# Kernel optimization log

Hardware: AMD Instinct MI355X
Metric: run time of the kernel (lower is better)

Reference implementation:

```python
import jax, jax.numpy as jnp
import numpy as np

NEG_SLOPE = 0.2

def gatv2(x, edge_index, Wl, bl, Wr, br, att, bias):
    # PyG GATv2Conv (share_weights=False, add_self_loops=True, concat=True)
    N = x.shape[0]
    H, D = att.shape
    src0, dst0 = edge_index[0], edge_index[1]
    # remove_self_loops + add_self_loops semantics: mask existing self loops,
    # append one self loop per node (keeps static shapes under jit)
    loop = jnp.arange(N, dtype=src0.dtype)
    src = jnp.concatenate([src0, loop])
    dst = jnp.concatenate([dst0, loop])
    keep = jnp.concatenate([src0 != dst0, jnp.ones(N, dtype=bool)])  # drop original i->i edges
    xl = (x @ Wl + bl).reshape(N, H, D)  # source-side transform
    xr = (x @ Wr + br).reshape(N, H, D)  # target-side transform
    e = xl[src] + xr[dst]                                  # [E,H,D]
    logits = jnp.einsum('ehd,hd->eh', jax.nn.leaky_relu(e, NEG_SLOPE), att)
    logits = jnp.where(keep[:, None], logits, -jnp.inf)
    m = jax.ops.segment_max(logits, dst, num_segments=N)   # [N,H]
    ex = jnp.where(keep[:, None], jnp.exp(logits - m[dst]), 0.0)
    denom = jax.ops.segment_sum(ex, dst, num_segments=N)   # [N,H]
    alpha = ex / (denom[dst] + 1e-16)                      # [E,H]
    out = jax.ops.segment_sum(alpha[..., None] * xl[src], dst, num_segments=N)
    return out.reshape(N, H * D) + bias

def setup_inputs() -> dict:
    key = jax.random.key(0)
    ks = jax.random.split(key, 20)
    N, E, F, Hd = 50000, 400000, 5, 128
    s = 0.05
    inp = {
        'x': jax.random.normal(ks[0], (N, F), dtype=jnp.float32),
        'edge_index': jax.random.randint(ks[1], (2, E), 0, N, dtype=jnp.int64),
        # node_embed MLP
        'W1': jax.random.normal(ks[2], (F, Hd), dtype=jnp.float32) * s,
        'b1': jnp.zeros((Hd,), jnp.float32),
        'W2': jax.random.normal(ks[3], (Hd, Hd), dtype=jnp.float32) * s,
        'b2': jnp.zeros((Hd,), jnp.float32),
        # gnn1: GATv2Conv(128 -> 128, heads=4)
        'Wl1': jax.random.normal(ks[4], (Hd, 4 * Hd), dtype=jnp.float32) * s,
        'bl1': jnp.zeros((4 * Hd,), jnp.float32),
        'Wr1': jax.random.normal(ks[5], (Hd, 4 * Hd), dtype=jnp.float32) * s,
        'br1': jnp.zeros((4 * Hd,), jnp.float32),
        'att1': jax.random.normal(ks[6], (4, Hd), dtype=jnp.float32) * s,
        'bias1': jnp.zeros((4 * Hd,), jnp.float32),
        # gnn2: GATv2Conv(512 -> 128, heads=1)
        'Wl2': jax.random.normal(ks[7], (4 * Hd, Hd), dtype=jnp.float32) * s,
        'bl2': jnp.zeros((Hd,), jnp.float32),
        'Wr2': jax.random.normal(ks[8], (4 * Hd, Hd), dtype=jnp.float32) * s,
        'br2': jnp.zeros((Hd,), jnp.float32),
        'att2': jax.random.normal(ks[9], (1, Hd), dtype=jnp.float32) * s,
        'bias2': jnp.zeros((Hd,), jnp.float32),
    }
    return inp

def reference(x, edge_index, W1, b1, W2, b2, Wl1, bl1, Wr1, br1, att1, bias1,
              Wl2, bl2, Wr2, br2, att2, bias2):
    h = jax.nn.relu(x @ W1 + b1) @ W2 + b2                 # node_embed MLP
    h = jax.nn.relu(gatv2(h, edge_index, Wl1, bl1, Wr1, br1, att1, bias1))
    out = gatv2(h, edge_index, Wl2, bl2, Wr2, br2, att2, bias2)
    return out  # [N, 128]
```

## Files before the change

kernel.cpp:

```cpp
#include <hip/hip_runtime.h>
#include <math.h>

typedef __attribute__((ext_vector_type(8))) short bf16x8;
typedef __attribute__((ext_vector_type(4))) float f32x4;
typedef unsigned short ushort;
typedef unsigned int uint;

static __device__ __forceinline__ ushort f2bf(float f) {
    unsigned u = __float_as_uint(f);
    u = u + 0x7fff + ((u >> 16) & 1);
    return (ushort)(u >> 16);
}
static __device__ __forceinline__ float bf2f(ushort h) {
    return __uint_as_float(((unsigned)h) << 16);
}

template <int CTRL>
static __device__ __forceinline__ float dpp_add(float c) {
    int p = __builtin_amdgcn_update_dpp(0, __float_as_int(c), CTRL, 0xf, 0xf, true);
    return c + __int_as_float(p);
}
static __device__ __forceinline__ float group16_sum(float c) {
    c = dpp_add<0xB1>(c);
    c = dpp_add<0x4E>(c);
    c = dpp_add<0x141>(c);
    c = dpp_add<0x140>(c);
    return c;
}


__global__ void k_fill(const int* __restrict__ src, const int* __restrict__ dst,
                       int E, int* __restrict__ counts, int* __restrict__ colA) {
    int i = blockIdx.x * blockDim.x + threadIdx.x;
    if (i < E) {
        int s = src[i], d = dst[i];
        if (s != d) {
            int p = atomicAdd(&counts[d], 1);
            if (p < 64) colA[(size_t)d * 64 + p] = s;
        }
    }
}


__global__ __launch_bounds__(256) void k_repack(
    const float* __restrict__ W2, const float* __restrict__ Wl1,
    const float* __restrict__ Wr1, const float* __restrict__ Wl2,
    const float* __restrict__ Wr2,
    ushort* __restrict__ wfh, ushort* __restrict__ wfl)
{
    int job = blockIdx.y;
    int t = blockIdx.x * 256 + threadIdx.x;
    int ks = t >> 9, n = (t >> 6) & 7, l = t & 63;

    const float* W; int ldw, rowoff, col0;
    if (job == 0)      { W = W2;  ldw = 128; rowoff = 0;              col0 = 0; }
    else if (job < 5)  { W = Wl1; ldw = 512; rowoff = 0;              col0 = (job - 1) * 128; }
    else if (job < 9)  { W = Wr1; ldw = 512; rowoff = 0;              col0 = (job - 5) * 128; }
    else if (job < 13) { W = Wl2; ldw = 128; rowoff = (job - 9) * 128;  col0 = 0; }
    else               { W = Wr2; ldw = 128; rowoff = (job - 13) * 128; col0 = 0; }

    int krow = rowoff + ks * 32 + (l >> 4) * 8;
    int col = col0 + n * 16 + (l & 15);
    size_t dbase = (size_t)job * 16384 + (((size_t)(ks * 8 + n)) * 64 + l) * 8;
#pragma unroll
    for (int j = 0; j < 8; j++) {
        float v = W[(size_t)(krow + j) * ldw + col];
        ushort h = f2bf(v);
        ushort lo = f2bf(v - bf2f(h));
        wfh[dbase + j] = h;
        wfl[dbase + j] = lo;
    }
}


__global__ __launch_bounds__(256) void k_mlp_h0(
    const float* __restrict__ x, const float* __restrict__ W1, const float* __restrict__ b1,
    const ushort* __restrict__ wfh, const ushort* __restrict__ wfl,
    const float* __restrict__ b2,
    ushort* __restrict__ C, int M)
{
    int tid = threadIdx.x;
    int w = tid >> 6, l = tid & 63;
    int m0 = blockIdx.x * 128 + w * 32;
    int lr = l & 15, kg = l >> 4;

    int row0 = m0 + lr, row1 = row0 + 16;
    bool ok0 = row0 < M, ok1 = row1 < M;

    float x0[5], x1[5];
#pragma unroll
    for (int k = 0; k < 5; k++) {
        x0[k] = ok0 ? x[(size_t)row0 * 5 + k] : 0.f;
        x1[k] = ok1 ? x[(size_t)row1 * 5 + k] : 0.f;
    }

    bf16x8 a0[4], a1[4];
#pragma unroll
    for (int ks = 0; ks < 4; ks++) {
#pragma unroll
        for (int j = 0; j < 8; j++) {
            int col = ks * 32 + kg * 8 + j;
            float wc[5];
#pragma unroll
            for (int k = 0; k < 5; k++) wc[k] = W1[k * 128 + col];
            float bb = b1[col];
            float h0v = bb, h1v = bb;
#pragma unroll
            for (int k = 0; k < 5; k++) {
                h0v = fmaf(x0[k], wc[k], h0v);
                h1v = fmaf(x1[k], wc[k], h1v);
            }
            a0[ks][j] = (short)f2bf(fmaxf(h0v, 0.f));
            a1[ks][j] = (short)f2bf(fmaxf(h1v, 0.f));
        }
    }

    f32x4 acc[2][8];
#pragma unroll
    for (int i = 0; i < 2; i++)
#pragma unroll
        for (int j = 0; j < 8; j++) acc[i][j] = (f32x4){0.f, 0.f, 0.f, 0.f};

#pragma unroll
    for (int ks = 0; ks < 4; ks++) {
#pragma unroll
        for (int n = 0; n < 8; n++) {
            size_t bo = (((size_t)(ks * 8 + n)) * 64 + l) * 8;
            bf16x8 bh = *(const bf16x8*)(wfh + bo);
            bf16x8 bl = *(const bf16x8*)(wfl + bo);
            acc[0][n] = __builtin_amdgcn_mfma_f32_16x16x32_bf16(a0[ks], bh, acc[0][n], 0, 0, 0);
            acc[0][n] = __builtin_amdgcn_mfma_f32_16x16x32_bf16(a0[ks], bl, acc[0][n], 0, 0, 0);
            acc[1][n] = __builtin_amdgcn_mfma_f32_16x16x32_bf16(a1[ks], bh, acc[1][n], 0, 0, 0);
            acc[1][n] = __builtin_amdgcn_mfma_f32_16x16x32_bf16(a1[ks], bl, acc[1][n], 0, 0, 0);
        }
    }

#pragma unroll
    for (int mf = 0; mf < 2; mf++) {
#pragma unroll
        for (int r = 0; r < 4; r++) {
            int row = m0 + mf * 16 + kg * 4 + r;
            if (row >= M) continue;
#pragma unroll
            for (int n = 0; n < 8; n++) {
                size_t idx = (size_t)row * 128 + n * 16 + lr;
                C[idx] = f2bf(acc[mf][n][r] + b2[n * 16 + lr]);
            }
        }
    }
}


__global__ __launch_bounds__(256) void gemm_xlr1(
    const ushort* __restrict__ A,
    const ushort* __restrict__ wh, const ushort* __restrict__ wl,
    const float* __restrict__ bl1, const float* __restrict__ br1,
    ushort* __restrict__ out, int M)
{
    int tid = threadIdx.x;
    int w = tid >> 6, l = tid & 63;
    int m0 = blockIdx.x * 128 + w * 32;
    int lr = l & 15, kg = l >> 4;

    int row0 = m0 + lr, row1 = row0 + 16;
    bool ok0 = row0 < M, ok1 = row1 < M;
    const bf16x8 zz = {0, 0, 0, 0, 0, 0, 0, 0};

    bf16x8 a0[4], a1[4];
#pragma unroll
    for (int ks = 0; ks < 4; ks++) {
        int koff = ks * 32 + kg * 8;
        a0[ks] = ok0 ? *(const bf16x8*)(A + (size_t)row0 * 128 + koff) : zz;
        a1[ks] = ok1 ? *(const bf16x8*)(A + (size_t)row1 * 128 + koff) : zz;
    }

    for (int t = 0; t < 8; t++) {
        const ushort* bh_base = wh + (size_t)t * 16384;
        const ushort* bl_base = wl + (size_t)t * 16384;

        f32x4 acc[2][8];
#pragma unroll
        for (int i = 0; i < 2; i++)
#pragma unroll
            for (int j = 0; j < 8; j++) acc[i][j] = (f32x4){0.f, 0.f, 0.f, 0.f};

#pragma unroll
        for (int ks = 0; ks < 4; ks++) {
#pragma unroll
            for (int n = 0; n < 8; n++) {
                size_t bo = (((size_t)(ks * 8 + n)) * 64 + l) * 8;
                bf16x8 bh = *(const bf16x8*)(bh_base + bo);
                bf16x8 bl = *(const bf16x8*)(bl_base + bo);
                acc[0][n] = __builtin_amdgcn_mfma_f32_16x16x32_bf16(a0[ks], bh, acc[0][n], 0, 0, 0);
                acc[0][n] = __builtin_amdgcn_mfma_f32_16x16x32_bf16(a0[ks], bl, acc[0][n], 0, 0, 0);
                acc[1][n] = __builtin_amdgcn_mfma_f32_16x16x32_bf16(a1[ks], bh, acc[1][n], 0, 0, 0);
                acc[1][n] = __builtin_amdgcn_mfma_f32_16x16x32_bf16(a1[ks], bl, acc[1][n], 0, 0, 0);
            }
        }

        float bcol[8];
#pragma unroll
        for (int n = 0; n < 8; n++)
            bcol[n] = (t < 4) ? bl1[t * 128 + n * 16 + lr] : br1[(t - 4) * 128 + n * 16 + lr];

#pragma unroll
        for (int mf = 0; mf < 2; mf++) {
#pragma unroll
            for (int r = 0; r < 4; r++) {
                int row = m0 + mf * 16 + kg * 4 + r;
                if (row >= M) continue;
#pragma unroll
                for (int n = 0; n < 8; n++)
                    out[(size_t)row * 1024 + t * 128 + n * 16 + lr] = f2bf(acc[mf][n][r] + bcol[n]);
            }
        }
    }
}


__global__ __launch_bounds__(256) void gemm_xlr2(
    const ushort* __restrict__ A,
    const ushort* __restrict__ wfh, const ushort* __restrict__ wfl,
    const float* __restrict__ bl2, const float* __restrict__ br2,
    ushort* __restrict__ xl2, ushort* __restrict__ xr2, int M)
{
    int tid = threadIdx.x;
    int w = tid >> 6, l = tid & 63;
    int m0 = blockIdx.x * 64 + w * 16;
    int lr = l & 15, kg = l >> 4;

    int row0 = m0 + lr;
    bool ok0 = row0 < M;
    const bf16x8 zz = {0, 0, 0, 0, 0, 0, 0, 0};

    f32x4 acc[2][8];
#pragma unroll
    for (int i = 0; i < 2; i++)
#pragma unroll
        for (int j = 0; j < 8; j++) acc[i][j] = (f32x4){0.f, 0.f, 0.f, 0.f};

    for (int kc = 0; kc < 4; kc++) {
        bf16x8 ah[4];
#pragma unroll
        for (int ks = 0; ks < 4; ks++)
            ah[ks] = ok0 ? *(const bf16x8*)(A + (size_t)row0 * 512 + kc * 128 + ks * 32 + kg * 8) : zz;

#pragma unroll
        for (int t = 0; t < 2; t++) {
            const ushort* bh_base = wfh + (size_t)(9 + t * 4 + kc) * 16384;
            const ushort* bl_base = wfl + (size_t)(9 + t * 4 + kc) * 16384;
#pragma unroll
            for (int ks = 0; ks < 4; ks++) {
#pragma unroll
                for (int n = 0; n < 8; n++) {
                    size_t bo = (((size_t)(ks * 8 + n)) * 64 + l) * 8;
                    bf16x8 bh = *(const bf16x8*)(bh_base + bo);
                    bf16x8 bl = *(const bf16x8*)(bl_base + bo);
                    acc[t][n] = __builtin_amdgcn_mfma_f32_16x16x32_bf16(ah[ks], bh, acc[t][n], 0, 0, 0);
                    acc[t][n] = __builtin_amdgcn_mfma_f32_16x16x32_bf16(ah[ks], bl, acc[t][n], 0, 0, 0);
                }
            }
        }
    }

#pragma unroll
    for (int r = 0; r < 4; r++) {
        int row = m0 + kg * 4 + r;
        if (row >= M) continue;
#pragma unroll
        for (int n = 0; n < 8; n++) {
            int col = n * 16 + lr;
            xl2[(size_t)row * 128 + col] = f2bf(acc[0][n][r] + bl2[col]);
            xr2[(size_t)row * 128 + col] = f2bf(acc[1][n][r] + br2[col]);
        }
    }
}


__global__ __launch_bounds__(256) void gat_edge4(
    const ushort* __restrict__ xlr,
    const float* __restrict__ att,
    const float* __restrict__ bias,
    const int* __restrict__ counts, const int* __restrict__ colA,
    ushort* __restrict__ h1,
    int N)
{
    int n = blockIdx.x;
    int h = threadIdx.x >> 6, l = threadIdx.x & 63;
    int g = l >> 4, q = l & 15;

    const ushort* xlbase = xlr + h * 128 + q * 8;

    bf16x8 xrv = *(const bf16x8*)(xlr + (size_t)n * 1024 + (4 + h) * 128 + q * 8);
    float4 ata = *(const float4*)(att + h * 128 + q * 8);
    float4 atb = *(const float4*)(att + h * 128 + q * 8 + 4);
    float xr[8] , at[8] = {ata.x, ata.y, ata.z, ata.w, atb.x, atb.y, atb.z, atb.w};
#pragma unroll
    for (int j = 0; j < 8; j++) xr[j] = bf2f((ushort)xrv[j]);

    auto dotc = [&](bf16x8 v8, float* vv) -> float {
        float c = 0.f;
#pragma unroll
        for (int j = 0; j < 8; j++) {
            vv[j] = bf2f((ushort)v8[j]);
            float t = vv[j] + xr[j];
            t = (t > 0.f) ? t : 0.2f * t;
            c = fmaf(t, at[j], c);
        }
        return group16_sum(c);
    };

    float selfv[8];
    bf16x8 vself = *(const bf16x8*)(xlbase + (size_t)n * 1024);
    float cs = dotc(vself, selfv);

    int cnt = min(counts[n], 64);
    const int* col = colA + (size_t)n * 64;

    float s = 0.f, o[8];
#pragma unroll
    for (int j = 0; j < 8; j++) o[j] = 0.f;

    auto edge = [&](bf16x8 v8) {
        float vv[8];
        float c = dotc(v8, vv);
        float p = __expf(fminf(c - cs, 80.f));
        s += p;
#pragma unroll
        for (int j = 0; j < 8; j++) o[j] = fmaf(p, vv[j], o[j]);
    };

    for (int base = g; base < cnt; base += 16) {
        int x0 = col[base];
        int x1 = (base + 4  < cnt) ? col[base + 4]  : -1;
        int x2 = (base + 8  < cnt) ? col[base + 8]  : -1;
        int x3 = (base + 12 < cnt) ? col[base + 12] : -1;
        int y1 = (x1 >= 0) ? x1 : n;
        int y2 = (x2 >= 0) ? x2 : n;
        int y3 = (x3 >= 0) ? x3 : n;
        bf16x8 v0 = *(const bf16x8*)(xlbase + (size_t)x0 * 1024);
        bf16x8 v1 = *(const bf16x8*)(xlbase + (size_t)y1 * 1024);
        bf16x8 v2 = *(const bf16x8*)(xlbase + (size_t)y2 * 1024);
        bf16x8 v3 = *(const bf16x8*)(xlbase + (size_t)y3 * 1024);
        edge(v0);
        if (x1 >= 0) edge(v1);
        if (x2 >= 0) edge(v2);
        if (x3 >= 0) edge(v3);
    }

#pragma unroll
    for (int off = 16; off <= 32; off <<= 1) {
        s += __shfl_xor(s, off);
#pragma unroll
        for (int j = 0; j < 8; j++) o[j] += __shfl_xor(o[j], off);
    }

    s += 1.f;
#pragma unroll
    for (int j = 0; j < 8; j++) o[j] += selfv[j];

    if (g == 0) {
        float inv = 1.f / (s + 1e-16f);
        float4 ba = *(const float4*)(bias + h * 128 + q * 8);
        float4 bb = *(const float4*)(bias + h * 128 + q * 8 + 4);
        float bs[8] = {ba.x, ba.y, ba.z, ba.w, bb.x, bb.y, bb.z, bb.w};
        bf16x8 pk;
#pragma unroll
        for (int j = 0; j < 8; j++)
            pk[j] = (short)f2bf(fmaxf(o[j] * inv + bs[j], 0.f));
        *(bf16x8*)(h1 + (size_t)n * 512 + h * 128 + q * 8) = pk;
    }
}


__global__ __launch_bounds__(256) void gat_edge1(
    const ushort* __restrict__ xl, const ushort* __restrict__ xr,
    const float* __restrict__ att, const float* __restrict__ bias,
    const int* __restrict__ counts, const int* __restrict__ colA,
    float* __restrict__ out, int N)
{
    int n = blockIdx.x * 4 + (threadIdx.x >> 6);
    if (n >= N) return;
    int l = threadIdx.x & 63;
    int g = l >> 4, q = l & 15;

    const ushort* xlbase = xl + q * 8;

    bf16x8 xrv = *(const bf16x8*)(xr + (size_t)n * 128 + q * 8);
    float4 ata = *(const float4*)(att + q * 8);
    float4 atb = *(const float4*)(att + q * 8 + 4);
    float xrr[8], at[8] = {ata.x, ata.y, ata.z, ata.w, atb.x, atb.y, atb.z, atb.w};
#pragma unroll
    for (int j = 0; j < 8; j++) xrr[j] = bf2f((ushort)xrv[j]);

    auto dotc = [&](bf16x8 v8, float* vv) -> float {
        float c = 0.f;
#pragma unroll
        for (int j = 0; j < 8; j++) {
            vv[j] = bf2f((ushort)v8[j]);
            float t = vv[j] + xrr[j];
            t = (t > 0.f) ? t : 0.2f * t;
            c = fmaf(t, at[j], c);
        }
        return group16_sum(c);
    };

    float selfv[8];
    bf16x8 vself = *(const bf16x8*)(xlbase + (size_t)n * 128);
    float cs = dotc(vself, selfv);

    int cnt = min(counts[n], 64);
    const int* col = colA + (size_t)n * 64;

    float s = 0.f, o[8];
#pragma unroll
    for (int j = 0; j < 8; j++) o[j] = 0.f;

    auto edge = [&](bf16x8 v8) {
        float vv[8];
        float c = dotc(v8, vv);
        float p = __expf(fminf(c - cs, 80.f));
        s += p;
#pragma unroll
        for (int j = 0; j < 8; j++) o[j] = fmaf(p, vv[j], o[j]);
    };

    for (int base = g; base < cnt; base += 16) {
        int x0 = col[base];
        int x1 = (base + 4  < cnt) ? col[base + 4]  : -1;
        int x2 = (base + 8  < cnt) ? col[base + 8]  : -1;
        int x3 = (base + 12 < cnt) ? col[base + 12] : -1;
        int y1 = (x1 >= 0) ? x1 : n;
        int y2 = (x2 >= 0) ? x2 : n;
        int y3 = (x3 >= 0) ? x3 : n;
        bf16x8 v0 = *(const bf16x8*)(xlbase + (size_t)x0 * 128);
        bf16x8 v1 = *(const bf16x8*)(xlbase + (size_t)y1 * 128);
        bf16x8 v2 = *(const bf16x8*)(xlbase + (size_t)y2 * 128);
        bf16x8 v3 = *(const bf16x8*)(xlbase + (size_t)y3 * 128);
        edge(v0);
        if (x1 >= 0) edge(v1);
        if (x2 >= 0) edge(v2);
        if (x3 >= 0) edge(v3);
    }

#pragma unroll
    for (int off = 16; off <= 32; off <<= 1) {
        s += __shfl_xor(s, off);
#pragma unroll
        for (int j = 0; j < 8; j++) o[j] += __shfl_xor(o[j], off);
    }

    s += 1.f;
#pragma unroll
    for (int j = 0; j < 8; j++) o[j] += selfv[j];

    if (g == 0) {
        float inv = 1.f / (s + 1e-16f);
        float4 ba = *(const float4*)(bias + q * 8);
        float4 bb = *(const float4*)(bias + q * 8 + 4);
        float4 r0, r1;
        r0.x = o[0] * inv + ba.x;  r0.y = o[1] * inv + ba.y;
        r0.z = o[2] * inv + ba.z;  r0.w = o[3] * inv + ba.w;
        r1.x = o[4] * inv + bb.x;  r1.y = o[5] * inv + bb.y;
        r1.z = o[6] * inv + bb.z;  r1.w = o[7] * inv + bb.w;
        *(float4*)(out + (size_t)n * 128 + q * 8)     = r0;
        *(float4*)(out + (size_t)n * 128 + q * 8 + 4) = r1;
    }
}


extern "C" void kernel_launch(void* const* d_in, const int* in_sizes, int n_in,
                              void* d_out, int out_size, void* d_ws, size_t ws_size,
                              hipStream_t stream) {
    const float* x    = (const float*)d_in[0];
    const int* ei     = (const int*)d_in[1];
    const float* W1   = (const float*)d_in[2];
    const float* b1   = (const float*)d_in[3];
    const float* W2   = (const float*)d_in[4];
    const float* b2   = (const float*)d_in[5];
    const float* Wl1  = (const float*)d_in[6];
    const float* bl1  = (const float*)d_in[7];
    const float* Wr1  = (const float*)d_in[8];
    const float* br1  = (const float*)d_in[9];
    const float* att1 = (const float*)d_in[10];
    const float* bias1= (const float*)d_in[11];
    const float* Wl2  = (const float*)d_in[12];
    const float* bl2  = (const float*)d_in[13];
    const float* Wr2  = (const float*)d_in[14];
    const float* br2  = (const float*)d_in[15];
    const float* att2 = (const float*)d_in[16];
    const float* bias2= (const float*)d_in[17];

    int E = in_sizes[1] / 2;
    int N = in_sizes[0] / 5;
    const int* srcE = ei;
    const int* dstE = ei + E;

    float* dout = (float*)d_out;

    ushort* xlr1 = (ushort*)d_ws;
    ushort* h1   = xlr1 + (size_t)N * 1024;
    ushort* h0   = h1 + (size_t)N * 512;
    ushort* xr2  = h0 + (size_t)N * 128;
    ushort* wfh  = xr2 + (size_t)N * 128;
    ushort* wfl  = wfh + 17 * 16384;
    int* counts = (int*)(wfl + 17 * 16384);
    int* colA   = counts + N;

    ushort* xl2 = h0;

    hipMemsetAsync(counts, 0, (size_t)N * sizeof(int), stream);
    k_fill<<<(E + 255) / 256, 256, 0, stream>>>(srcE, dstE, E, counts, colA);

    {
        dim3 g(8, 17);
        k_repack<<<g, 256, 0, stream>>>(W2, Wl1, Wr1, Wl2, Wr2, wfh, wfl);
    }

    int mb128 = (N + 127) / 128;
    int mb64  = (N + 63) / 64;

    k_mlp_h0<<<mb128, 256, 0, stream>>>(x, W1, b1, wfh, wfl, b2, h0, N);

    gemm_xlr1<<<mb128, 256, 0, stream>>>(h0, wfh + 16384, wfl + 16384, bl1, br1, xlr1, N);
    gat_edge4<<<N, 256, 0, stream>>>(xlr1, att1, bias1, counts, colA, h1, N);

    gemm_xlr2<<<mb64, 256, 0, stream>>>(h1, wfh, wfl, bl2, br2, xl2, xr2, N);
    gat_edge1<<<(N + 3) / 4, 256, 0, stream>>>(xl2, xr2, att2, bias2, counts, colA, dout, N);
}
```

Measured before the change: 343.8 us.

## Split leaky-ReLU attention logit into abs term plus precomputed per-node dot

Uses the identity leaky_relu(t) = 0.6t + 0.4|t| to rewrite the attention logit. The linear source-side part, 0.6·att·xl, is computed once per node in the GEMM epilogues and stored to small dav buffers. The target-side linear part cancels in the softmax, so it is dropped. Each edge now needs only a fabs-based FMA dot instead of compare, select and multiply, at the cost of an extra scattered 4-byte load per edge and a cross-lane reduction in the GEMM epilogue.

```diff
diff --git a/kernel.cpp b/kernel.cpp
--- a/kernel.cpp
+++ b/kernel.cpp
@@ -155,7 +155,8 @@
     const ushort* __restrict__ A,
     const ushort* __restrict__ wh, const ushort* __restrict__ wl,
     const float* __restrict__ bl1, const float* __restrict__ br1,
-    ushort* __restrict__ out, int M)
+    const float* __restrict__ att,
+    ushort* __restrict__ out, float* __restrict__ dav1, int M)
 {
     int tid = threadIdx.x;
     int w = tid >> 6, l = tid & 63;
@@ -203,15 +204,38 @@
         for (int n = 0; n < 8; n++)
             bcol[n] = (t < 4) ? bl1[t * 128 + n * 16 + lr] : br1[(t - 4) * 128 + n * 16 + lr];
 
-#pragma unroll
-        for (int mf = 0; mf < 2; mf++) {
-#pragma unroll
-            for (int r = 0; r < 4; r++) {
-                int row = m0 + mf * 16 + kg * 4 + r;
-                if (row >= M) continue;
-#pragma unroll
-                for (int n = 0; n < 8; n++)
-                    out[(size_t)row * 1024 + t * 128 + n * 16 + lr] = f2bf(acc[mf][n][r] + bcol[n]);
+        if (t < 4) {
+            float at6[8];
+#pragma unroll
+            for (int n = 0; n < 8; n++) at6[n] = 0.6f * att[t * 128 + n * 16 + lr];
+#pragma unroll
+            for (int mf = 0; mf < 2; mf++) {
+#pragma unroll
+                for (int r = 0; r < 4; r++) {
+                    int row = m0 + mf * 16 + kg * 4 + r;
+                    if (row >= M) continue;
+                    float partial = 0.f;
+#pragma unroll
+                    for (int n = 0; n < 8; n++) {
+                        float v = acc[mf][n][r] + bcol[n];
+                        partial = fmaf(at6[n], v, partial);
+                        out[(size_t)row * 1024 + t * 128 + n * 16 + lr] = f2bf(v);
+                    }
+                    float red = group16_sum(partial);
+                    if (lr == 0) dav1[(size_t)row * 4 + t] = red;
+                }
+            }
+        } else {
+#pragma unroll
+            for (int mf = 0; mf < 2; mf++) {
+#pragma unroll
+                for (int r = 0; r < 4; r++) {
+                    int row = m0 + mf * 16 + kg * 4 + r;
+                    if (row >= M) continue;
+#pragma unroll
+                    for (int n = 0; n < 8; n++)
+                        out[(size_t)row * 1024 + t * 128 + n * 16 + lr] = f2bf(acc[mf][n][r] + bcol[n]);
+                }
             }
         }
     }
@@ -222,7 +246,9 @@
     const ushort* __restrict__ A,
     const ushort* __restrict__ wfh, const ushort* __restrict__ wfl,
     const float* __restrict__ bl2, const float* __restrict__ br2,
-    ushort* __restrict__ xl2, ushort* __restrict__ xr2, int M)
+    const float* __restrict__ att,
+    ushort* __restrict__ xl2, ushort* __restrict__ xr2,
+    float* __restrict__ dav2, int M)
 {
     int tid = threadIdx.x;
     int w = tid >> 6, l = tid & 63;
@@ -263,16 +289,25 @@
         }
     }
 
+    float at6[8];
+#pragma unroll
+    for (int n = 0; n < 8; n++) at6[n] = 0.6f * att[n * 16 + lr];
+
 #pragma unroll
     for (int r = 0; r < 4; r++) {
         int row = m0 + kg * 4 + r;
         if (row >= M) continue;
+        float partial = 0.f;
 #pragma unroll
         for (int n = 0; n < 8; n++) {
             int col = n * 16 + lr;
-            xl2[(size_t)row * 128 + col] = f2bf(acc[0][n][r] + bl2[col]);
+            float vl = acc[0][n][r] + bl2[col];
+            partial = fmaf(at6[n], vl, partial);
+            xl2[(size_t)row * 128 + col] = f2bf(vl);
             xr2[(size_t)row * 128 + col] = f2bf(acc[1][n][r] + br2[col]);
         }
+        float red = group16_sum(partial);
+        if (lr == 0) dav2[row] = red;
     }
 }
 
@@ -282,8 +317,8 @@
     const float* __restrict__ att,
     const float* __restrict__ bias,
     const int* __restrict__ counts, const int* __restrict__ colA,
-    ushort* __restrict__ h1,
-    int N)
+    const float* __restrict__ dav1,
+    ushort* __restrict__ h1, int N)
 {
     int n = blockIdx.x;
     int h = threadIdx.x >> 6, l = threadIdx.x & 63;
@@ -294,25 +329,25 @@
     bf16x8 xrv = *(const bf16x8*)(xlr + (size_t)n * 1024 + (4 + h) * 128 + q * 8);
     float4 ata = *(const float4*)(att + h * 128 + q * 8);
     float4 atb = *(const float4*)(att + h * 128 + q * 8 + 4);
-    float xr[8] , at[8] = {ata.x, ata.y, ata.z, ata.w, atb.x, atb.y, atb.z, atb.w};
+    float xr[8], at4[8] = {0.4f*ata.x, 0.4f*ata.y, 0.4f*ata.z, 0.4f*ata.w,
+                           0.4f*atb.x, 0.4f*atb.y, 0.4f*atb.z, 0.4f*atb.w};
 #pragma unroll
     for (int j = 0; j < 8; j++) xr[j] = bf2f((ushort)xrv[j]);
 
-    auto dotc = [&](bf16x8 v8, float* vv) -> float {
+    auto absdot = [&](bf16x8 v8, float* vv) -> float {
         float c = 0.f;
 #pragma unroll
         for (int j = 0; j < 8; j++) {
             vv[j] = bf2f((ushort)v8[j]);
             float t = vv[j] + xr[j];
-            t = (t > 0.f) ? t : 0.2f * t;
-            c = fmaf(t, at[j], c);
+            c = fmaf(at4[j], fabsf(t), c);
         }
         return group16_sum(c);
     };
 
     float selfv[8];
     bf16x8 vself = *(const bf16x8*)(xlbase + (size_t)n * 1024);
-    float cs = dotc(vself, selfv);
+    float cs = absdot(vself, selfv) + dav1[(size_t)n * 4 + h];
 
     int cnt = min(counts[n], 64);
     const int* col = colA + (size_t)n * 64;
@@ -321,9 +356,9 @@
 #pragma unroll
     for (int j = 0; j < 8; j++) o[j] = 0.f;
 
-    auto edge = [&](bf16x8 v8) {
+    auto edge = [&](bf16x8 v8, float dv) {
         float vv[8];
-        float c = dotc(v8, vv);
+        float c = absdot(v8, vv) + dv;
         float p = __expf(fminf(c - cs, 80.f));
         s += p;
 #pragma unroll
@@ -342,10 +377,14 @@
         bf16x8 v1 = *(const bf16x8*)(xlbase + (size_t)y1 * 1024);
         bf16x8 v2 = *(const bf16x8*)(xlbase + (size_t)y2 * 1024);
         bf16x8 v3 = *(const bf16x8*)(xlbase + (size_t)y3 * 1024);
-        edge(v0);
-        if (x1 >= 0) edge(v1);
-        if (x2 >= 0) edge(v2);
-        if (x3 >= 0) edge(v3);
+        float d0 = dav1[(size_t)x0 * 4 + h];
+        float d1 = dav1[(size_t)y1 * 4 + h];
+        float d2 = dav1[(size_t)y2 * 4 + h];
+        float d3 = dav1[(size_t)y3 * 4 + h];
+        edge(v0, d0);
+        if (x1 >= 0) edge(v1, d1);
+        if (x2 >= 0) edge(v2, d2);
+        if (x3 >= 0) edge(v3, d3);
     }
 
 #pragma unroll
@@ -377,6 +416,7 @@
     const ushort* __restrict__ xl, const ushort* __restrict__ xr,
     const float* __restrict__ att, const float* __restrict__ bias,
     const int* __restrict__ counts, const int* __restrict__ colA,
+    const float* __restrict__ dav2,
     float* __restrict__ out, int N)
 {
     int n = blockIdx.x * 4 + (threadIdx.x >> 6);
@@ -389,25 +429,25 @@
     bf16x8 xrv = *(const bf16x8*)(xr + (size_t)n * 128 + q * 8);
     float4 ata = *(const float4*)(att + q * 8);
     float4 atb = *(const float4*)(att + q * 8 + 4);
-    float xrr[8], at[8] = {ata.x, ata.y, ata.z, ata.w, atb.x, atb.y, atb.z, atb.w};
+    float xrr[8], at4[8] = {0.4f*ata.x, 0.4f*ata.y, 0.4f*ata.z, 0.4f*ata.w,
+                            0.4f*atb.x, 0.4f*atb.y, 0.4f*atb.z, 0.4f*atb.w};
 #pragma unroll
     for (int j = 0; j < 8; j++) xrr[j] = bf2f((ushort)xrv[j]);
 
-    auto dotc = [&](bf16x8 v8, float* vv) -> float {
+    auto absdot = [&](bf16x8 v8, float* vv) -> float {
         float c = 0.f;
 #pragma unroll
         for (int j = 0; j < 8; j++) {
             vv[j] = bf2f((ushort)v8[j]);
             float t = vv[j] + xrr[j];
-            t = (t > 0.f) ? t : 0.2f * t;
-            c = fmaf(t, at[j], c);
+            c = fmaf(at4[j], fabsf(t), c);
         }
         return group16_sum(c);
     };
 
     float selfv[8];
     bf16x8 vself = *(const bf16x8*)(xlbase + (size_t)n * 128);
-    float cs = dotc(vself, selfv);
+    float cs = absdot(vself, selfv) + dav2[n];
 
     int cnt = min(counts[n], 64);
     const int* col = colA + (size_t)n * 64;
@@ -416,9 +456,9 @@
 #pragma unroll
     for (int j = 0; j < 8; j++) o[j] = 0.f;
 
-    auto edge = [&](bf16x8 v8) {
+    auto edge = [&](bf16x8 v8, float dv) {
         float vv[8];
-        float c = dotc(v8, vv);
+        float c = absdot(v8, vv) + dv;
         float p = __expf(fminf(c - cs, 80.f));
         s += p;
 #pragma unroll
@@ -437,10 +477,14 @@
         bf16x8 v1 = *(const bf16x8*)(xlbase + (size_t)y1 * 128);
         bf16x8 v2 = *(const bf16x8*)(xlbase + (size_t)y2 * 128);
         bf16x8 v3 = *(const bf16x8*)(xlbase + (size_t)y3 * 128);
-        edge(v0);
-        if (x1 >= 0) edge(v1);
-        if (x2 >= 0) edge(v2);
-        if (x3 >= 0) edge(v3);
+        float d0 = dav2[x0];
+        float d1 = dav2[y1];
+        float d2 = dav2[y2];
+        float d3 = dav2[y3];
+        edge(v0, d0);
+        if (x1 >= 0) edge(v1, d1);
+        if (x2 >= 0) edge(v2, d2);
+        if (x3 >= 0) edge(v3, d3);
     }
 
 #pragma unroll
@@ -506,6 +550,8 @@
     ushort* wfl  = wfh + 17 * 16384;
     int* counts = (int*)(wfl + 17 * 16384);
     int* colA   = counts + N;
+    float* dav1 = (float*)(colA + (size_t)N * 64);
+    float* dav2 = dav1 + (size_t)N * 4;
 
     ushort* xl2 = h0;
 
@@ -522,9 +568,10 @@
 
     k_mlp_h0<<<mb128, 256, 0, stream>>>(x, W1, b1, wfh, wfl, b2, h0, N);
 
-    gemm_xlr1<<<mb128, 256, 0, stream>>>(h0, wfh + 16384, wfl + 16384, bl1, br1, xlr1, N);
-    gat_edge4<<<N, 256, 0, stream>>>(xlr1, att1, bias1, counts, colA, h1, N);
-
-    gemm_xlr2<<<mb64, 256, 0, stream>>>(h1, wfh, wfl, bl2, br2, xl2, xr2, N);
-    gat_edge1<<<(N + 3) / 4, 256, 0, stream>>>(xl2, xr2, att2, bias2, counts, colA, dout, N);
-}
+    gemm_xlr1<<<mb128, 256, 0, stream>>>(h0, wfh + 16384, wfl + 16384, bl1, br1, att1,
+                                         xlr1, dav1, N);
+    gat_edge4<<<N, 256, 0, stream>>>(xlr1, att1, bias1, counts, colA, dav1, h1, N);
+
+    gemm_xlr2<<<mb64, 256, 0, stream>>>(h1, wfh, wfl, bl2, br2, att2, xl2, xr2, dav2, N);
+    gat_edge1<<<(N + 3) / 4, 256, 0, stream>>>(xl2, xr2, att2, bias2, counts, colA, dav2, dout, N);
+}
```

After: 359.3 us. +4.5%, slower.
